# Optimization experiments

Measured on AMD Instinct MI355X. Metric: run time of the kernel, lower is better.

## Reference

```python
import jax, jax.numpy as jnp
import numpy as np

IMG = 512
STRIDES = (8.0, 16.0, 32.0)   # p3, p4, p5
ROI = 7                        # roi_size
SR = 2                         # roi_align sampling ratio (fixed; torchvision default -1 is adaptive)
IOU_LOW, IOU_HIGH = 0.4, 0.6   # fg/bg matching thresholds (2nd-stage)
NUM_CLASSES = 20
B, R, M, C = 4, 256, 40, 256


def _make_boxes(key, b, n, max_wh):
    k1, k2 = jax.random.split(key)
    cxy = jax.random.uniform(k1, (b, n, 2), minval=0.0, maxval=float(IMG))
    wh = jax.random.uniform(k2, (b, n, 2), minval=16.0, maxval=float(max_wh))
    x1y1 = jnp.clip(cxy - wh / 2, 0.0, IMG - 1.0)
    x2y2 = jnp.clip(cxy + wh / 2, x1y1 + 1.0, float(IMG))
    return jnp.concatenate([x1y1, x2y2], axis=-1)


def setup_inputs() -> dict:
    key = jax.random.key(0)
    ks = jax.random.split(key, 12)
    feats_p3 = jax.random.normal(ks[0], (B, C, 64, 64), jnp.float32)
    feats_p4 = jax.random.normal(ks[1], (B, C, 32, 32), jnp.float32)
    feats_p5 = jax.random.normal(ks[2], (B, C, 16, 16), jnp.float32)
    props_p3 = _make_boxes(ks[3], B, R, 128)
    props_p4 = _make_boxes(ks[4], B, R, 256)
    props_p5 = _make_boxes(ks[5], B, R, 512)
    gt_xyxy = _make_boxes(ks[6], B, M, 400)
    gt_cls = jax.random.randint(ks[7], (B, M, 1), 0, NUM_CLASSES).astype(jnp.float32)
    gt = jnp.concatenate([gt_xyxy, gt_cls], axis=-1)
    pad = (jnp.arange(M) >= 25)[None, :, None]   # last 15 rows are padding (class -1)
    gt_boxes = jnp.where(pad, -1.0, gt)
    conv_w = jax.random.normal(ks[8], (C, C, 3, 3), jnp.float32) * 0.01
    conv_b = jnp.zeros((C,), jnp.float32)
    fc_w = jax.random.normal(ks[9], (NUM_CLASSES + 1, C * ROI * ROI), jnp.float32) * 0.01
    fc_b = jnp.zeros((NUM_CLASSES + 1,), jnp.float32)
    return {"feats_p3": feats_p3, "feats_p4": feats_p4, "feats_p5": feats_p5,
            "props_p3": props_p3, "props_p4": props_p4, "props_p5": props_p5,
            "gt_boxes": gt_boxes, "conv_w": conv_w, "conv_b": conv_b,
            "fc_w": fc_w, "fc_b": fc_b}


def _bilinear(feat, ys, xs):
    # feat: (C,H,W); ys: (R,G,1); xs: (R,1,G) -> (C,R,G,G)
    Cc, H, W = feat.shape
    valid = (ys >= -1.0) & (ys <= H) & (xs >= -1.0) & (xs <= W)
    y = jnp.clip(ys, 0.0, H - 1.0)
    x = jnp.clip(xs, 0.0, W - 1.0)
    y0f = jnp.floor(y); x0f = jnp.floor(x)
    y0 = y0f.astype(jnp.int32); x0 = x0f.astype(jnp.int32)
    y1 = jnp.minimum(y0 + 1, H - 1); x1 = jnp.minimum(x0 + 1, W - 1)
    ly = y - y0f; lx = x - x0f
    hy = 1.0 - ly; hx = 1.0 - lx
    v = (feat[:, y0, x0] * (hy * hx) + feat[:, y0, x1] * (hy * lx)
         + feat[:, y1, x0] * (ly * hx) + feat[:, y1, x1] * (ly * lx))
    return jnp.where(valid, v, 0.0)


def _roi_align(feat, rois, scale):
    # feat: (C,H,W); rois: (R,4) xyxy in image coords; aligned=True
    r = rois.shape[0]
    x1 = rois[:, 0] * scale - 0.5
    y1 = rois[:, 1] * scale - 0.5
    roi_w = rois[:, 2] * scale - 0.5 - x1
    roi_h = rois[:, 3] * scale - 0.5 - y1
    G = ROI * SR
    frac = (jnp.arange(G, dtype=feat.dtype) + 0.5) / G
    xs = x1[:, None] + frac[None, :] * roi_w[:, None]   # (R,G)
    ys = y1[:, None] + frac[None, :] * roi_h[:, None]
    v = _bilinear(feat, ys[:, :, None], xs[:, None, :])  # (C,R,G,G)
    v = v.transpose(1, 0, 2, 3).reshape(r, -1, ROI, SR, ROI, SR)
    return v.mean(axis=(3, 5))                            # (R,C,7,7)


def _iou(b1, b2):
    # b1: (N,4), b2: (M,4) -> (N,M)
    tl = jnp.maximum(b1[:, None, :2], b2[None, :, :2])
    br = jnp.minimum(b1[:, None, 2:4], b2[None, :, 2:4])
    inter = jnp.clip(br - tl, 0.0).prod(-1)
    a1 = (b1[:, 2:4] - b1[:, :2]).prod(-1)
    a2 = (b2[:, 2:4] - b2[:, :2]).prod(-1)
    return inter / (a1[:, None] + a2[None, :] - inter)


def _match(props, gt):
    # props: (N,4); gt: (M,5) padded with class -1
    valid = gt[:, 4] != -1
    m = jnp.where(valid[None, :], _iou(props, gt[:, :4]), -1.0)
    q = m.max(axis=1)
    matched = gt[m.argmax(axis=1)]                       # (N,5)
    matched = jnp.where((q <= IOU_LOW)[:, None], -1.0, matched)      # background
    matched = jnp.where(((q > IOU_LOW) & (q < IOU_HIGH))[:, None], -1e8, matched)  # neutral
    return matched


def reference(feats_p3, feats_p4, feats_p5, props_p3, props_p4, props_p5,
              gt_boxes, conv_w, conv_b, fc_w, fc_b):
    levels = [(feats_p3, props_p3, STRIDES[0]),
              (feats_p4, props_p4, STRIDES[1]),
              (feats_p5, props_p5, STRIDES[2])]
    # ROI-align every proposal at its level; order: image-major, then level, then roi
    per_level = [jax.vmap(lambda f, p, s=s: _roi_align(f, p, 1.0 / s))(f, p)
                 for f, p, s in levels]                   # each (B,R,C,7,7)
    roi_feats = jnp.stack(per_level, axis=1).reshape(-1, C, ROI, ROI)
    # cls head: conv3x3 + relu + flatten + linear
    h = jax.lax.conv_general_dilated(roi_feats, conv_w, (1, 1), 'SAME')
    h = jax.nn.relu(h + conv_b[None, :, None, None])
    logits = h.reshape(h.shape[0], -1) @ fc_w.T + fc_b    # (B*3*R, num_classes+1)
    # match concatenated per-image proposals to GT (no-grad pipeline)
    props_all = jnp.concatenate([props_p3, props_p4, props_p5], axis=1)  # (B,3R,4)
    matched = jax.vmap(_match)(jax.lax.stop_gradient(props_all), gt_boxes)
    return logits, matched
```

## Files before the change

kernel.cpp:

```cpp
#include <hip/hip_runtime.h>

typedef unsigned short ushort_t;
typedef __attribute__((ext_vector_type(4))) unsigned short ushort4_t;
typedef __attribute__((ext_vector_type(8))) short short8;
typedef __attribute__((ext_vector_type(4))) unsigned int uint4v;
typedef __attribute__((ext_vector_type(2))) float float2v;
typedef __attribute__((ext_vector_type(4))) float floatx4;
typedef __attribute__((ext_vector_type(16))) float floatx16;

#define B_ 4
#define C_ 256
#define R_ 256
#define M_ 40
#define NCLS 21
#define ROI_ 7
#define G_ 14
#define NROI_TOT 3072
#define PROPS_PER_IMG 768
#define POOL_PITCH 264
#define WCONV_ELEMS (256 * 2304)
#define NKB 392
#define WFC2_ELEMS (NKB * 32 * 32)
#define OFF_FWB   WCONV_ELEMS
#define OFF_CL3   (OFF_FWB + WFC2_ELEMS)
#define OFF_CL4   (OFF_CL3 + 4 * 64 * 64 * 256)
#define OFF_CL5   (OFF_CL4 + 4 * 32 * 32 * 256)

__device__ __forceinline__ ushort_t f2bf(float f) {
  unsigned u = __builtin_bit_cast(unsigned, f);
  u += 0x7fff + ((u >> 16) & 1);
  return (ushort_t)(u >> 16);
}
__device__ __forceinline__ float bf2f(ushort_t h) {
  unsigned u = ((unsigned)h) << 16;
  return __builtin_bit_cast(float, u);
}
__device__ __forceinline__ float2v cvt2(unsigned u) {
  float2v r;
  r[0] = __builtin_bit_cast(float, u << 16);
  r[1] = __builtin_bit_cast(float, u & 0xffff0000u);
  return r;
}

__global__ __launch_bounds__(256) void prep_kernel(
    const float* __restrict__ cw, const float* __restrict__ fw,
    const float* __restrict__ f3, const float* __restrict__ f4,
    const float* __restrict__ f5, const float* __restrict__ p3,
    const float* __restrict__ p4, const float* __restrict__ p5,
    const float* __restrict__ gt, ushort_t* __restrict__ wr,
    ushort_t* __restrict__ fwb, ushort_t* __restrict__ cl3,
    ushort_t* __restrict__ cl4, ushort_t* __restrict__ cl5,
    float* __restrict__ out) {
  __shared__ ushort_t tile[64 * 257];
  const int id = blockIdx.x;
  const int t = threadIdx.x;

  if (id < 512) {
    const int i0 = id * 256 + t;
    const int stride = 512 * 256;
    for (int idx = i0; idx < WCONV_ELEMS; idx += stride) {
      const int kk = idx >> 12;
      const int rem = idx & 4095;
      const int co = rem >> 4;
      const int i = rem & 15;
      const int k = kk * 16 + i;
      const int j = k >> 8;
      const int ci = k & 255;
      wr[idx] = f2bf(cw[(co * 256 + ci) * 9 + j]);
    }
    for (int idx = i0; idx < WFC2_ELEMS; idx += stride) {
      const int kb = idx >> 10;
      const int rem = idx & 1023;
      const int cls = rem >> 5;
      const int koff = rem & 31;
      fwb[idx] =
          (cls < NCLS) ? f2bf(fw[(size_t)cls * 12544 + kb * 32 + koff]) : 0;
    }
  } else if (id < 960) {
    const int fid = id - 512;
    const float* in;
    ushort_t* outp;
    int b, y, W;
    if (fid < 256) { in = f3; outp = cl3; W = 64; b = fid >> 6; y = fid & 63; }
    else if (fid < 384) { in = f4; outp = cl4; W = 32; b = (fid - 256) >> 5; y = (fid - 256) & 31; }
    else { in = f5; outp = cl5; W = 16; b = (fid - 384) >> 4; y = (fid - 384) & 15; }

    for (int idx = t; idx < 256 * W; idx += 256) {
      const int c = idx / W;
      const int x = idx - c * W;
      tile[x * 257 + c] = f2bf(in[((size_t)(b * 256 + c) * W + y) * W + x]);
    }
    __syncthreads();
    ushort_t* orow = outp + ((size_t)(b * W + y) * W) * 256;
    for (int idx = t; idx < W * 64; idx += 256) {
      const int x = idx >> 6;
      const int c4 = (idx & 63) * 4;
      ushort4_t v;
      v[0] = tile[x * 257 + c4 + 0];
      v[1] = tile[x * 257 + c4 + 1];
      v[2] = tile[x * 257 + c4 + 2];
      v[3] = tile[x * 257 + c4 + 3];
      *(ushort4_t*)(orow + (size_t)x * 256 + c4) = v;
    }
  } else {
    const int gidx = (id - 960) * 256 + t;
    if (gidx >= NROI_TOT) return;
    const int b = gidx / PROPS_PER_IMG;
    const int i = gidx - b * PROPS_PER_IMG;
    const int lvl = i >> 8;
    const int r = i & 255;
    const float* prop =
        (lvl == 0 ? p3 : (lvl == 1 ? p4 : p5)) + (size_t)(b * R_ + r) * 4;
    const float px1 = prop[0], py1 = prop[1], px2 = prop[2], py2 = prop[3];
    const float a1 = (px2 - px1) * (py2 - py1);
    const float* gtb = gt + (size_t)b * M_ * 5;

    float best = -2.f;
    int bi = 0;
    for (int j = 0; j < M_; ++j) {
      const float gx1 = gtb[j * 5 + 0], gy1 = gtb[j * 5 + 1];
      const float gx2 = gtb[j * 5 + 2], gy2 = gtb[j * 5 + 3];
      const float cls = gtb[j * 5 + 4];
      const float tlx = fmaxf(px1, gx1), tly = fmaxf(py1, gy1);
      const float brx = fminf(px2, gx2), bry = fminf(py2, gy2);
      const float iw = fmaxf(brx - tlx, 0.f), ih = fmaxf(bry - tly, 0.f);
      const float inter = iw * ih;
      const float a2 = (gx2 - gx1) * (gy2 - gy1);
      const float iou = inter / ((a1 + a2) - inter);
      const float m = (cls != -1.0f) ? iou : -1.0f;
      if (m > best) { best = m; bi = j; }
    }
    float o0, o1, o2, o3, o4;
    if (best <= 0.4f) {
      o0 = o1 = o2 = o3 = o4 = -1.0f;
    } else if (best < 0.6f) {
      o0 = o1 = o2 = o3 = o4 = -1e8f;
    } else {
      o0 = gtb[bi * 5 + 0]; o1 = gtb[bi * 5 + 1]; o2 = gtb[bi * 5 + 2];
      o3 = gtb[bi * 5 + 3]; o4 = gtb[bi * 5 + 4];
    }
    float* od = out + (size_t)NROI_TOT * NCLS + (size_t)gidx * 5;
    od[0] = o0; od[1] = o1; od[2] = o2; od[3] = o3; od[4] = o4;
  }
}

__global__ __launch_bounds__(512, 4) void cls_head_kernel(
    const ushort_t* __restrict__ cl3, const ushort_t* __restrict__ cl4,
    const ushort_t* __restrict__ cl5, const float* __restrict__ p3,
    const float* __restrict__ p4, const float* __restrict__ p5,
    const ushort_t* __restrict__ wr, const float* __restrict__ conv_b,
    const ushort_t* __restrict__ fwb, const float* __restrict__ fc_b,
    float* __restrict__ out) {
  __shared__ __align__(16) ushort_t s_pool[2 * 50 * POOL_PITCH];
  __shared__ int s_iy0[28], s_iy1[28], s_ix0[28], s_ix1[28];
  __shared__ float s_ly[28], s_lx[28], s_vy[28], s_vx[28];
  __shared__ float s_fcred[512];

  const int bid = blockIdx.x;
  const int t = threadIdx.x;

  const int img = (bid & 7) >> 1;
  const int pair = (bid >> 3) * 2 + (bid & 1);
  const int rid0 = img * PROPS_PER_IMG + pair * 2;

  const ushort_t* clb_[2];
  int W_[2];
  const float* prop_[2];
#pragma unroll
  for (int rr = 0; rr < 2; ++rr) {
    const int rid = rid0 + rr;
    const int b = rid / PROPS_PER_IMG;
    const int rem = rid - b * PROPS_PER_IMG;
    const int lvl = rem >> 8;
    const int r = rem & 255;
    const ushort_t* base;
    const float* pp;
    int Wl;
    if (lvl == 0) { base = cl3; pp = p3; Wl = 64; }
    else if (lvl == 1) { base = cl4; pp = p4; Wl = 32; }
    else { base = cl5; pp = p5; Wl = 16; }
    clb_[rr] = base + (size_t)b * Wl * Wl * 256;
    W_[rr] = Wl;
    prop_[rr] = pp + (size_t)(b * R_ + r) * 4;
  }

  if (t < POOL_PITCH) {
    s_pool[49 * POOL_PITCH + t] = 0;
    s_pool[99 * POOL_PITCH + t] = 0;
  }

  if (t < 56) {
    const int rr = t / 28;
    const int tt = t - rr * 28;
    const float* prop = prop_[rr];
    const int H = W_[rr];
    const float scale = 1.0f / (float)(H == 64 ? 8 : (H == 32 ? 16 : 32));
    const float bx1 = prop[0], by1 = prop[1], bx2 = prop[2], by2 = prop[3];
    const float ax = bx1 * scale - 0.5f;
    const float ay = by1 * scale - 0.5f;
    const float rw = bx2 * scale - 0.5f - ax;
    const float rh = by2 * scale - 0.5f - ay;
    const int i = (tt < G_) ? tt : (tt - G_);
    const float frac = ((float)i + 0.5f) / (float)G_;
    const int o = rr * G_ + i;
    if (tt < G_) {
      float yy = ay + frac * rh;
      float v = (yy >= -1.0f && yy <= (float)H) ? 1.0f : 0.0f;
      float y = fminf(fmaxf(yy, 0.0f), (float)(H - 1));
      float y0f = floorf(y);
      int y0 = (int)y0f;
      s_iy0[o] = y0;
      s_iy1[o] = min(y0 + 1, H - 1);
      s_ly[o] = y - y0f;
      s_vy[o] = v;
    } else {
      float xx = ax + frac * rw;
      float v = (xx >= -1.0f && xx <= (float)H) ? 1.0f : 0.0f;
      float x = fminf(fmaxf(xx, 0.0f), (float)(H - 1));
      float x0f = floorf(x);
      int x0 = (int)x0f;
      s_ix0[o] = x0;
      s_ix1[o] = min(x0 + 1, H - 1);
      s_lx[o] = x - x0f;
      s_vx[o] = v;
    }
  }
  __syncthreads();

  const int l = t & 63;
  const int w = t >> 6;

  {
    const int hw = l >> 5;
    const int c8 = (l & 31) * 8;
    for (int cb = w * 2; cb < 98; cb += 16) {
      const int cell = cb + hw;
      if (cell >= 98) continue;
      const int rr = (cell >= 49) ? 1 : 0;
      const int pos = cell - rr * 49;
      const int py = pos / 7, px = pos - (pos / 7) * 7;
      const ushort_t* clb = clb_[rr];
      const int W = W_[rr];
      float2v a01 = {0.f, 0.f}, a23 = {0.f, 0.f};
      float2v a45 = {0.f, 0.f}, a67 = {0.f, 0.f};
#pragma unroll
      for (int sy = 0; sy < 2; ++sy) {
        const int gy = rr * G_ + 2 * py + sy;
        const int iy0 = s_iy0[gy], iy1 = s_iy1[gy];
        const float ly = s_ly[gy], vy = s_vy[gy];
        const float hy = 1.0f - ly;
#pragma unroll
        for (int sx = 0; sx < 2; ++sx) {
          const int gx = rr * G_ + 2 * px + sx;
          const int ix0 = s_ix0[gx], ix1 = s_ix1[gx];
          const float lx = s_lx[gx], vx = s_vx[gx];
          const float hx = 1.0f - lx;
          const float vv = vy * vx;
          const float w00 = vv * hy * hx, w01 = vv * hy * lx;
          const float w10 = vv * ly * hx, w11 = vv * ly * lx;
          const uint4v u00 = *(const uint4v*)(clb + ((size_t)(iy0 * W + ix0) * 256 + c8));
          const uint4v u01 = *(const uint4v*)(clb + ((size_t)(iy0 * W + ix1) * 256 + c8));
          const uint4v u10 = *(const uint4v*)(clb + ((size_t)(iy1 * W + ix0) * 256 + c8));
          const uint4v u11 = *(const uint4v*)(clb + ((size_t)(iy1 * W + ix1) * 256 + c8));
          a01 += cvt2(u00[0]) * w00 + cvt2(u01[0]) * w01 +
                 cvt2(u10[0]) * w10 + cvt2(u11[0]) * w11;
          a23 += cvt2(u00[1]) * w00 + cvt2(u01[1]) * w01 +
                 cvt2(u10[1]) * w10 + cvt2(u11[1]) * w11;
          a45 += cvt2(u00[2]) * w00 + cvt2(u01[2]) * w01 +
                 cvt2(u10[2]) * w10 + cvt2(u11[2]) * w11;
          a67 += cvt2(u00[3]) * w00 + cvt2(u01[3]) * w01 +
                 cvt2(u10[3]) * w10 + cvt2(u11[3]) * w11;
        }
      }
      short8 pv;
      pv[0] = (short)f2bf(a01[0] * 0.25f);
      pv[1] = (short)f2bf(a01[1] * 0.25f);
      pv[2] = (short)f2bf(a23[0] * 0.25f);
      pv[3] = (short)f2bf(a23[1] * 0.25f);
      pv[4] = (short)f2bf(a45[0] * 0.25f);
      pv[5] = (short)f2bf(a45[1] * 0.25f);
      pv[6] = (short)f2bf(a67[0] * 0.25f);
      pv[7] = (short)f2bf(a67[1] * 0.25f);
      *(short8*)&s_pool[(rr * 50 + pos) * POOL_PITCH + c8] = pv;
    }
  }
  __syncthreads();

  const int ml = l & 31;
  const int quad = l >> 5;
  const int co_base = w * 32;

  const int pA = ml;
  const int pB = ml + 32;
  const int pyA = pA / 7, pxA = pA % 7;
  const int pyB = pB / 7, pxB = pB % 7;

  floatx16 acc[4];
#pragma unroll
  for (int a = 0; a < 4; ++a)
#pragma unroll
    for (int i = 0; i < 16; ++i) acc[a][i] = 0.f;

  const ushort_t* a0p = wr + (co_base + ml) * 16 + quad * 8;

  int kk = 0;
  for (int j = 0; j < 9; ++j) {
    const int dy = j / 3 - 1, dx = j % 3 - 1;
    int bnA, bnB;
    {
      const int ry = pyA + dy, rx = pxA + dx;
      const bool ok = (ry >= 0) & (ry < 7) & (rx >= 0) & (rx < 7);
      bnA = ok ? ry * 7 + rx : 49;
    }
    {
      const int ry = pyB + dy, rx = pxB + dx;
      const bool ok = (pB < 49) & (ry >= 0) & (ry < 7) & (rx >= 0) & (rx < 7);
      bnB = ok ? ry * 7 + rx : 49;
    }
    const int row0 = bnA, row1 = bnB, row2 = 50 + bnA, row3 = 50 + bnB;

#pragma unroll 4
    for (int kc = 0; kc < 16; ++kc, ++kk) {
      const short8 a0 = *(const short8*)(a0p + kk * 4096);
      const int cof = kc * 16 + quad * 8;
      const short8 b0 = *(const short8*)&s_pool[row0 * POOL_PITCH + cof];
      const short8 b1 = *(const short8*)&s_pool[row1 * POOL_PITCH + cof];
      const short8 b2 = *(const short8*)&s_pool[row2 * POOL_PITCH + cof];
      const short8 b3 = *(const short8*)&s_pool[row3 * POOL_PITCH + cof];
      acc[0] = __builtin_amdgcn_mfma_f32_32x32x16_bf16(a0, b0, acc[0], 0, 0, 0);
      acc[1] = __builtin_amdgcn_mfma_f32_32x32x16_bf16(a0, b1, acc[1], 0, 0, 0);
      acc[2] = __builtin_amdgcn_mfma_f32_32x32x16_bf16(a0, b2, acc[2], 0, 0, 0);
      acc[3] = __builtin_amdgcn_mfma_f32_32x32x16_bf16(a0, b3, acc[3], 0, 0, 0);
    }
  }
  __syncthreads();

  ushort_t* h_lds = s_pool;
#pragma unroll
  for (int reg = 0; reg < 16; ++reg) {
    const int co = co_base + (reg & 3) + 8 * (reg >> 2) + 4 * quad;
    const float cb = conv_b[co];
    const int base = co * 49;
    h_lds[base + pA] = f2bf(fmaxf(acc[0][reg] + cb, 0.f));
    h_lds[12544 + base + pA] = f2bf(fmaxf(acc[2][reg] + cb, 0.f));
    if (pB < 49) {
      h_lds[base + pB] = f2bf(fmaxf(acc[1][reg] + cb, 0.f));
      h_lds[12544 + base + pB] = f2bf(fmaxf(acc[3][reg] + cb, 0.f));
    }
  }
  __syncthreads();

  {
    const int n = l & 15;
    const int kq = l >> 4;
    const ushort_t* ap0 = fwb + (n * 4 + kq) * 8;
    const ushort_t* ap1 = ap0 + 512;
    const ushort_t* bp = h_lds + (size_t)(l & 1) * 12544 + kq * 8;
    const int kb0 = w * 49;

    floatx4 fa0, fa1;
#pragma unroll
    for (int i = 0; i < 4; ++i) { fa0[i] = 0.f; fa1[i] = 0.f; }

    for (int it = 0; it < 49; ++it) {
      const int kb = kb0 + it;
      const short8 av0 = *(const short8*)(ap0 + kb * 1024);
      const short8 av1 = *(const short8*)(ap1 + kb * 1024);
      const short8 bv = *(const short8*)(bp + kb * 32);
      fa0 = __builtin_amdgcn_mfma_f32_16x16x32_bf16(av0, bv, fa0, 0, 0, 0);
      fa1 = __builtin_amdgcn_mfma_f32_16x16x32_bf16(av1, bv, fa1, 0, 0, 0);
    }
    if (n < 2) {
      const int m4 = kq * 4;
#pragma unroll
      for (int reg = 0; reg < 4; ++reg) {
        s_fcred[((m4 + reg) * 2 + n) * 8 + w] = fa0[reg];
        s_fcred[((16 + m4 + reg) * 2 + n) * 8 + w] = fa1[reg];
      }
    }
  }
  __syncthreads();
  if (t < 2 * NCLS) {
    const int cls = t >> 1;
    const int rr = t & 1;
    const float* pr = &s_fcred[(cls * 2 + rr) * 8];
    float s = pr[0] + pr[1] + pr[2] + pr[3] + pr[4] + pr[5] + pr[6] + pr[7];
    out[(size_t)(rid0 + rr) * NCLS + cls] = s + fc_b[cls];
  }
}

extern "C" void kernel_launch(void* const* d_in, const int* in_sizes, int n_in,
                              void* d_out, int out_size, void* d_ws,
                              size_t ws_size, hipStream_t stream) {
  const float* f3 = (const float*)d_in[0];
  const float* f4 = (const float*)d_in[1];
  const float* f5 = (const float*)d_in[2];
  const float* p3 = (const float*)d_in[3];
  const float* p4 = (const float*)d_in[4];
  const float* p5 = (const float*)d_in[5];
  const float* gt = (const float*)d_in[6];
  const float* cw = (const float*)d_in[7];
  const float* cb = (const float*)d_in[8];
  const float* fw = (const float*)d_in[9];
  const float* fb = (const float*)d_in[10];
  float* out = (float*)d_out;

  ushort_t* wsp = (ushort_t*)d_ws;
  ushort_t* wr = wsp;
  ushort_t* fwb = wsp + OFF_FWB;
  ushort_t* cl3 = wsp + OFF_CL3;
  ushort_t* cl4 = wsp + OFF_CL4;
  ushort_t* cl5 = wsp + OFF_CL5;

  prep_kernel<<<972, 256, 0, stream>>>(cw, fw, f3, f4, f5, p3, p4, p5, gt, wr,
                                       fwb, cl3, cl4, cl5, out);
  cls_head_kernel<<<NROI_TOT / 2, 512, 0, stream>>>(cl3, cl4, cl5, p3, p4, p5,
                                                    wr, cb, fwb, fb, out);
}
```

Before: 368.8 us.

## Split conv MFMA work per wave by output channels and ROI; retile transpose LDS

```diff
diff --git a/kernel.cpp b/kernel.cpp
--- a/kernel.cpp
+++ b/kernel.cpp
@@ -51,7 +51,7 @@
     ushort_t* __restrict__ fwb, ushort_t* __restrict__ cl3,
     ushort_t* __restrict__ cl4, ushort_t* __restrict__ cl5,
     float* __restrict__ out) {
-  __shared__ ushort_t tile[64 * 257];
+  __shared__ ushort_t tile[256 * 65];
   const int id = blockIdx.x;
   const int t = threadIdx.x;
 
@@ -88,7 +88,7 @@
     for (int idx = t; idx < 256 * W; idx += 256) {
       const int c = idx / W;
       const int x = idx - c * W;
-      tile[x * 257 + c] = f2bf(in[((size_t)(b * 256 + c) * W + y) * W + x]);
+      tile[c * 65 + x] = f2bf(in[((size_t)(b * 256 + c) * W + y) * W + x]);
     }
     __syncthreads();
     ushort_t* orow = outp + ((size_t)(b * W + y) * W) * 256;
@@ -96,10 +96,10 @@
       const int x = idx >> 6;
       const int c4 = (idx & 63) * 4;
       ushort4_t v;
-      v[0] = tile[x * 257 + c4 + 0];
-      v[1] = tile[x * 257 + c4 + 1];
-      v[2] = tile[x * 257 + c4 + 2];
-      v[3] = tile[x * 257 + c4 + 3];
+      v[0] = tile[(c4 + 0) * 65 + x];
+      v[1] = tile[(c4 + 1) * 65 + x];
+      v[2] = tile[(c4 + 2) * 65 + x];
+      v[3] = tile[(c4 + 3) * 65 + x];
       *(ushort4_t*)(orow + (size_t)x * 256 + c4) = v;
     }
   } else {
@@ -154,7 +154,7 @@
   __shared__ __align__(16) ushort_t s_pool[2 * 50 * POOL_PITCH];
   __shared__ int s_iy0[28], s_iy1[28], s_ix0[28], s_ix1[28];
   __shared__ float s_ly[28], s_lx[28], s_vy[28], s_vx[28];
-  __shared__ float s_fcred[512];
+  __shared__ float s_fcred[NCLS * 2 * 8];
 
   const int bid = blockIdx.x;
   const int t = threadIdx.x;
@@ -184,7 +184,7 @@
     prop_[rr] = pp + (size_t)(b * R_ + r) * 4;
   }
 
-  if (t < POOL_PITCH) {
+  if (t < 256) {
     s_pool[49 * POOL_PITCH + t] = 0;
     s_pool[99 * POOL_PITCH + t] = 0;
   }
@@ -288,7 +288,9 @@
 
   const int ml = l & 31;
   const int quad = l >> 5;
-  const int co_base = w * 32;
+  const int cog = w & 3;
+  const int posg = w >> 2;
+  const int co_base = cog * 64;
 
   const int pA = ml;
   const int pB = ml + 32;
@@ -302,6 +304,8 @@
     for (int i = 0; i < 16; ++i) acc[a][i] = 0.f;
 
   const ushort_t* a0p = wr + (co_base + ml) * 16 + quad * 8;
+  const ushort_t* a1p = a0p + 32 * 16;
+  const int roff = posg * 50;
 
   int kk = 0;
   for (int j = 0; j < 9; ++j) {
@@ -317,35 +321,38 @@
       const bool ok = (pB < 49) & (ry >= 0) & (ry < 7) & (rx >= 0) & (rx < 7);
       bnB = ok ? ry * 7 + rx : 49;
     }
-    const int row0 = bnA, row1 = bnB, row2 = 50 + bnA, row3 = 50 + bnB;
+    const int row0 = roff + bnA, row1 = roff + bnB;
 
 #pragma unroll 4
     for (int kc = 0; kc < 16; ++kc, ++kk) {
       const short8 a0 = *(const short8*)(a0p + kk * 4096);
+      const short8 a1 = *(const short8*)(a1p + kk * 4096);
       const int cof = kc * 16 + quad * 8;
       const short8 b0 = *(const short8*)&s_pool[row0 * POOL_PITCH + cof];
       const short8 b1 = *(const short8*)&s_pool[row1 * POOL_PITCH + cof];
-      const short8 b2 = *(const short8*)&s_pool[row2 * POOL_PITCH + cof];
-      const short8 b3 = *(const short8*)&s_pool[row3 * POOL_PITCH + cof];
       acc[0] = __builtin_amdgcn_mfma_f32_32x32x16_bf16(a0, b0, acc[0], 0, 0, 0);
       acc[1] = __builtin_amdgcn_mfma_f32_32x32x16_bf16(a0, b1, acc[1], 0, 0, 0);
-      acc[2] = __builtin_amdgcn_mfma_f32_32x32x16_bf16(a0, b2, acc[2], 0, 0, 0);
-      acc[3] = __builtin_amdgcn_mfma_f32_32x32x16_bf16(a0, b3, acc[3], 0, 0, 0);
+      acc[2] = __builtin_amdgcn_mfma_f32_32x32x16_bf16(a1, b0, acc[2], 0, 0, 0);
+      acc[3] = __builtin_amdgcn_mfma_f32_32x32x16_bf16(a1, b1, acc[3], 0, 0, 0);
     }
   }
   __syncthreads();
 
   ushort_t* h_lds = s_pool;
-#pragma unroll
-  for (int reg = 0; reg < 16; ++reg) {
-    const int co = co_base + (reg & 3) + 8 * (reg >> 2) + 4 * quad;
-    const float cb = conv_b[co];
-    const int base = co * 49;
-    h_lds[base + pA] = f2bf(fmaxf(acc[0][reg] + cb, 0.f));
-    h_lds[12544 + base + pA] = f2bf(fmaxf(acc[2][reg] + cb, 0.f));
-    if (pB < 49) {
-      h_lds[base + pB] = f2bf(fmaxf(acc[1][reg] + cb, 0.f));
-      h_lds[12544 + base + pB] = f2bf(fmaxf(acc[3][reg] + cb, 0.f));
+  {
+    const int hoff = posg * 12544;
+#pragma unroll
+    for (int af = 0; af < 2; ++af) {
+#pragma unroll
+      for (int reg = 0; reg < 16; ++reg) {
+        const int co = co_base + af * 32 + (reg & 3) + 8 * (reg >> 2) + 4 * quad;
+        const float cb = conv_b[co];
+        const int base = hoff + co * 49;
+        h_lds[base + pA] = f2bf(fmaxf(acc[af * 2 + 0][reg] + cb, 0.f));
+        if (pB < 49) {
+          h_lds[base + pB] = f2bf(fmaxf(acc[af * 2 + 1][reg] + cb, 0.f));
+        }
+      }
     }
   }
   __syncthreads();
@@ -374,8 +381,10 @@
       const int m4 = kq * 4;
 #pragma unroll
       for (int reg = 0; reg < 4; ++reg) {
-        s_fcred[((m4 + reg) * 2 + n) * 8 + w] = fa0[reg];
-        s_fcred[((16 + m4 + reg) * 2 + n) * 8 + w] = fa1[reg];
+        const int cls0 = m4 + reg;
+        const int cls1 = 16 + m4 + reg;
+        s_fcred[(cls0 * 2 + n) * 8 + w] = fa0[reg];
+        if (cls1 < NCLS) s_fcred[(cls1 * 2 + n) * 8 + w] = fa1[reg];
       }
     }
   }
```

Result: slower. 403.8 us (+9.5%).
